# Kernel tuning notes

Measured on AMD Instinct MI355X. Metric: run time of the kernel, lower is better.

Reference implementation:

```python
import jax, jax.numpy as jnp
import numpy as np

N = 50000      # nodes
E = 800000     # edges
NF = 16        # nfeature_dim
H = 128        # hidden_dim
OUT = 4        # output_dim


def _edge_conv(x, edge_index, W1, b1, W2, b2, aggr):
    """PyG EdgeConv: message = MLP(cat[x_i, x_j - x_i]) per edge, aggregate at target i.
    edge_index[0]=source j, edge_index[1]=target i."""
    src, dst = edge_index[0], edge_index[1]
    xi = x[dst]                                   # [E, F]
    xj = x[src]                                   # [E, F]
    h = jnp.concatenate([xi, xj - xi], axis=-1)   # [E, 2F]
    m = jax.nn.relu(h @ W1 + b1) @ W2 + b2        # [E, H]
    if aggr == 'max':
        out = jax.ops.segment_max(m, dst, num_segments=N)
        out = jnp.where(jnp.isfinite(out), out, 0.0)  # nodes with no in-edges -> 0
    else:  # mean
        s = jax.ops.segment_sum(m, dst, num_segments=N)
        cnt = jax.ops.segment_sum(jnp.ones((m.shape[0], 1), m.dtype), dst, num_segments=N)
        out = s / jnp.maximum(cnt, 1.0)
    return out


def setup_inputs() -> dict:
    key = jax.random.key(0)
    ks = jax.random.split(key, 20)
    s = 0.05
    inp = {
        'x': jax.random.normal(ks[0], (N, NF), dtype=jnp.float32),
        'edge_attr': jax.random.uniform(ks[1], (E, 1), dtype=jnp.float32) + 0.1,
        'edge_index': jax.random.randint(ks[2], (2, E), 0, N, dtype=jnp.int64),
        # conv0: Linear(2*NF->H), Linear(H->H)
        'W01': jax.random.normal(ks[3], (2 * NF, H), dtype=jnp.float32) * s,
        'b01': jnp.zeros((H,), jnp.float32),
        'W02': jax.random.normal(ks[4], (H, H), dtype=jnp.float32) * s,
        'b02': jnp.zeros((H,), jnp.float32),
        # conv1: Linear(2*H->H), Linear(H->H)
        'W11': jax.random.normal(ks[5], (2 * H, H), dtype=jnp.float32) * s,
        'b11': jnp.zeros((H,), jnp.float32),
        'W12': jax.random.normal(ks[6], (H, H), dtype=jnp.float32) * s,
        'b12': jnp.zeros((H,), jnp.float32),
        # conv2: Linear(2*H->H), Linear(H->H)
        'W21': jax.random.normal(ks[7], (2 * H, H), dtype=jnp.float32) * s,
        'b21': jnp.zeros((H,), jnp.float32),
        'W22': jax.random.normal(ks[8], (H, H), dtype=jnp.float32) * s,
        'b22': jnp.zeros((H,), jnp.float32),
        # final fc
        'Wf': jax.random.normal(ks[9], (H, OUT), dtype=jnp.float32) * s,
        'bf': jnp.zeros((OUT,), jnp.float32),
    }
    return inp


def reference(x, edge_attr, edge_index, W01, b01, W02, b02, W11, b11, W12, b12,
              W21, b21, W22, b22, Wf, bf):
    # edge_attr is only nan-checked in the original forward; unused in math.
    # dropout_rate = 0.0 -> identity (eval-mode reference).
    h = _edge_conv(x, edge_index, W01, b01, W02, b02, 'max')
    h = jax.nn.relu(h)
    h = _edge_conv(h, edge_index, W11, b11, W12, b12, 'mean')
    h = jax.nn.relu(h)
    h = _edge_conv(h, edge_index, W21, b21, W22, b22, 'mean')
    return h @ Wf + bf  # [N, OUT]
```

## Files before the change

### kernel.cpp

```cpp
#include <hip/hip_runtime.h>
#include <stdint.h>

#define NNODES 50000
#define NEDGES 800000
#define FDIM 16
#define HDIM 128
#define NPAD 50176
#define NCH 98
#define NBLK64 782

typedef __attribute__((ext_vector_type(8))) short short8;
typedef __attribute__((ext_vector_type(4))) float f32x4;

static constexpr size_t NH  = (size_t)NNODES * HDIM;
static constexpr size_t NHB = NH * sizeof(float);

static constexpr size_t OFF_ENC   = 0;
static constexpr size_t OFF_PA    = NHB;
static constexpr size_t OFF_PB    = OFF_PA + NH * 2;
static constexpr size_t OFF_QA    = OFF_PB + NH * 2;
static constexpr size_t OFF_QB    = OFF_QA + NH * 2;
static constexpr size_t OFF_CNT   = OFF_QB + NH * 2;
static constexpr size_t OFF_CUR   = OFF_CNT + NPAD * 4;
static constexpr size_t OFF_CSUM  = OFF_CUR + NPAD * 4;
static constexpr size_t OFF_COFF  = OFF_CSUM + 512;
static constexpr size_t OFF_WFOLD = OFF_COFF + 512;
static constexpr size_t OFF_BFOLD = OFF_WFOLD + 2048;
static constexpr size_t OFF_FLAG  = OFF_BFOLD + 256;
static constexpr size_t OFF_SEDGE = OFF_FLAG + 256;
static constexpr size_t OFF_W02H  = OFF_SEDGE + (size_t)NEDGES * 8;
static constexpr size_t OFF_W02L  = OFF_W02H + 32768;
static constexpr size_t OFF_W12H  = OFF_W02L + 32768;
static constexpr size_t OFF_W12L  = OFF_W12H + 32768;
static constexpr size_t OFF_W11H  = OFF_W12L + 32768;
static constexpr size_t OFF_W11L  = OFF_W11H + 65536;
static constexpr size_t OFF_W21H  = OFF_W11L + 65536;
static constexpr size_t OFF_W21L  = OFF_W21H + 65536;

__device__ inline unsigned enc_f32(float m) {
  unsigned u = __float_as_uint(m);
  return (u & 0x80000000u) ? ~u : (u | 0x80000000u);
}

__device__ inline ushort bf16_rne(float v) {
  const unsigned u = __float_as_uint(v);
  return (ushort)((u + 0x7fffu + ((u >> 16) & 1u)) >> 16);
}

__device__ inline void bf16_split(float v, ushort& h, ushort& l) {
  unsigned u = __float_as_uint(v);
  unsigned hb = (u + 0x7fffu + ((u >> 16) & 1u)) & 0xffff0000u;
  h = (ushort)(hb >> 16);
  float r = v - __uint_as_float(hb);
  unsigned ur = __float_as_uint(r);
  l = (ushort)((ur + 0x7fffu + ((ur >> 16) & 1u)) >> 16);
}

__device__ inline short8 cvtpk8_bf16(const float v[8]) {
  unsigned r[4];
  #pragma unroll
  for (int k = 0; k < 4; ++k)
    asm("v_cvt_pk_bf16_f32 %0, %1, %2" : "=v"(r[k]) : "v"(v[2 * k]), "v"(v[2 * k + 1]));
  return *(short8*)r;
}

__device__ inline unsigned cvtpk_bf16(float a, float b) {
  unsigned r;
  asm("v_cvt_pk_bf16_f32 %0, %1, %2" : "=v"(r) : "v"(a), "v"(b));
  return r;
}

__global__ __launch_bounds__(256) void k_init(const int* __restrict__ raw,
                                              int* __restrict__ flag,
                                              unsigned* __restrict__ cnt,
                                              unsigned* __restrict__ outenc) {
  const int i = blockIdx.x * 256 + threadIdx.x;
  outenc[i] = 0u;
  if (i < NPAD) cnt[i] = 0u;
  if (i == 0) {
    int is64 = 1;
    #pragma unroll
    for (int k = 1; k < 64; k += 2)
      if (raw[k] != 0) is64 = 0;
    *flag = is64;
  }
}

__global__ __launch_bounds__(256) void k_count(const int* __restrict__ raw,
                                               const int* __restrict__ flag,
                                               unsigned* __restrict__ cnt) {
  const size_t e = (size_t)blockIdx.x * 256 + threadIdx.x;
  const int d = (*flag) ? raw[2 * ((size_t)NEDGES + e)] : raw[NEDGES + e];
  atomicAdd(&cnt[d], 1u);
}

__global__ __launch_bounds__(256) void k_scan1(const unsigned* __restrict__ cnt,
                                               unsigned* __restrict__ csum) {
  __shared__ unsigned s[256];
  const int t = threadIdx.x, b = blockIdx.x;
  s[t] = cnt[b * 512 + t] + cnt[b * 512 + 256 + t];
  __syncthreads();
  for (int off = 128; off; off >>= 1) {
    if (t < off) s[t] += s[t + off];
    __syncthreads();
  }
  if (t == 0) csum[b] = s[0];
}

__global__ void k_scan2(const unsigned* __restrict__ csum,
                        unsigned* __restrict__ coff) {
  if (threadIdx.x == 0) {
    unsigned r = 0;
    for (int i = 0; i < NCH; ++i) { coff[i] = r; r += csum[i]; }
  }
}

__global__ __launch_bounds__(256) void k_scan3(const unsigned* __restrict__ cnt,
                                               const unsigned* __restrict__ coff,
                                               unsigned* __restrict__ cursor) {
  __shared__ unsigned s[256];
  const int t = threadIdx.x, b = blockIdx.x;
  const int base = b * 512;
  const unsigned c0 = cnt[base + 2 * t], c1 = cnt[base + 2 * t + 1];
  s[t] = c0 + c1;
  __syncthreads();
  for (int off = 1; off < 256; off <<= 1) {
    unsigned v = s[t];
    if (t >= off) v += s[t - off];
    __syncthreads();
    s[t] = v;
    __syncthreads();
  }
  const unsigned o = coff[b] + s[t] - (c0 + c1);
  cursor[base + 2 * t] = o;
  cursor[base + 2 * t + 1] = o + c0;
}

__global__ __launch_bounds__(256) void k_scatter(const int* __restrict__ raw,
                                                 const int* __restrict__ flag,
                                                 unsigned* __restrict__ cursor,
                                                 int2* __restrict__ sedge) {
  const size_t e = (size_t)blockIdx.x * 256 + threadIdx.x;
  int s, d;
  if (*flag) { s = raw[2 * e]; d = raw[2 * ((size_t)NEDGES + e)]; }
  else       { s = raw[e];     d = raw[NEDGES + e]; }
  const unsigned p = atomicAdd(&cursor[d], 1u);
  int2 sd; sd.x = s; sd.y = d;
  sedge[p] = sd;
}

__device__ inline void prepw_body(const float* __restrict__ W2,
                                  ushort* __restrict__ Whi,
                                  ushort* __restrict__ Wlo, int blk) {
  const int gid = blk * 256 + threadIdx.x;
  const int row = gid & 15;
  const int kg  = (gid >> 4) & 3;
  const int ks  = (gid >> 6) & 3;
  const int ct  = gid >> 8;
  const int col = ct * 16 + row;
  const int k0  = ks * 32 + kg * 8;
  short8 hv, lv;
  #pragma unroll
  for (int j = 0; j < 8; ++j) {
    ushort h, l;
    bf16_split(W2[(size_t)(k0 + j) * HDIM + col], h, l);
    hv[j] = (short)h; lv[j] = (short)l;
  }
  *(short8*)(Whi + (size_t)gid * 8) = hv;
  *(short8*)(Wlo + (size_t)gid * 8) = lv;
}

__device__ inline void packab_body(const float* __restrict__ W1,
                                   ushort* __restrict__ Whi,
                                   ushort* __restrict__ Wlo, int blk) {
  const int gid = blk * 256 + threadIdx.x;
  const int row = gid & 15;
  const int kg  = (gid >> 4) & 3;
  const int ks  = (gid >> 6) & 3;
  const int ct  = gid >> 8;
  const int col = ct * 16 + row;
  const int k0  = ks * 32 + kg * 8;
  short8 hv, lv;
  #pragma unroll
  for (int j = 0; j < 8; ++j) {
    const int k = k0 + j;
    float v;
    if (col < HDIM) v = W1[(size_t)k * HDIM + col] - W1[(size_t)(k + HDIM) * HDIM + col];
    else            v = W1[(size_t)(k + HDIM) * HDIM + (col - HDIM)];
    ushort h, l;
    bf16_split(v, h, l);
    hv[j] = (short)h; lv[j] = (short)l;
  }
  *(short8*)(Whi + (size_t)gid * 8) = hv;
  *(short8*)(Wlo + (size_t)gid * 8) = lv;
}

__global__ __launch_bounds__(256) void k_prep_all(
    const float* __restrict__ W02, const float* __restrict__ W12,
    const float* __restrict__ W11, const float* __restrict__ W21,
    const float* __restrict__ W22, const float* __restrict__ Wf,
    const float* __restrict__ b22, const float* __restrict__ bf,
    ushort* __restrict__ W02h, ushort* __restrict__ W02l,
    ushort* __restrict__ W12h, ushort* __restrict__ W12l,
    ushort* __restrict__ W11h, ushort* __restrict__ W11l,
    ushort* __restrict__ W21h, ushort* __restrict__ W21l,
    float* __restrict__ Wfold, float* __restrict__ bfold) {
  const int b = blockIdx.x;
  if (b < 8)       prepw_body(W02, W02h, W02l, b);
  else if (b < 16) prepw_body(W12, W12h, W12l, b - 8);
  else if (b < 32) packab_body(W11, W11h, W11l, b - 16);
  else if (b < 48) packab_body(W21, W21h, W21l, b - 32);
  else {
    const int t = (b - 48) * 256 + threadIdx.x;
    const int f = t >> 2, o = t & 3;
    float acc = 0.f;
    for (int h = 0; h < HDIM; ++h)
      acc = fmaf(W22[f * HDIM + h], Wf[h * 4 + o], acc);
    Wfold[t] = acc;
    if (t < 4) {
      float a = bf[t];
      for (int h = 0; h < HDIM; ++h) a = fmaf(b22[h], Wf[h * 4 + t], a);
      bfold[t] = a;
    }
  }
}

__global__ __launch_bounds__(256) void k_node_ab16(const float* __restrict__ x,
                                                   const float* __restrict__ W1,
                                                   const float* __restrict__ b1,
                                                   ushort* __restrict__ Ab,
                                                   ushort* __restrict__ Bb) {
  __shared__ float s_x[16 * FDIM];
  const int tid = threadIdx.x;
  const int nb = blockIdx.x * 16;
  s_x[tid] = x[(size_t)nb * FDIM + tid];
  __syncthreads();
  const int h = tid & 127;
  const int half = tid >> 7;
  float accA[8], accB[8];
  #pragma unroll
  for (int j = 0; j < 8; ++j) { accA[j] = 0.f; accB[j] = 0.f; }
  #pragma unroll 4
  for (int f = 0; f < FDIM; ++f) {
    const float wt = W1[f * HDIM + h];
    const float wb = W1[(f + FDIM) * HDIM + h];
    const float wd = wt - wb;
    #pragma unroll
    for (int j = 0; j < 8; ++j) {
      const float xv = s_x[(half * 8 + j) * FDIM + f];
      accA[j] = fmaf(xv, wd, accA[j]);
      accB[j] = fmaf(xv, wb, accB[j]);
    }
  }
  const float bias = b1[h];
  #pragma unroll
  for (int j = 0; j < 8; ++j) {
    const size_t idx = (size_t)(nb + half * 8 + j) * HDIM + h;
    Ab[idx] = bf16_rne(accA[j] + bias);
    Bb[idx] = bf16_rne(accB[j]);
  }
}

__global__ __launch_bounds__(256) void k_node_ab_mfma(
    const unsigned* __restrict__ X, const ushort* __restrict__ Whi,
    const ushort* __restrict__ Wlo, const float* __restrict__ b1,
    ushort* __restrict__ Ab, ushort* __restrict__ Bb) {
  __shared__ __align__(16) ushort s_t[64 * 128];
  const int tid = threadIdx.x;
  const int nb = blockIdx.x * 64;

  #pragma unroll
  for (int it = 0; it < 4; ++it) {
    const int idx = tid + it * 256;
    const int row = idx >> 4;
    const int kg8 = idx & 15;
    const int n = nb + row;
    float v[8];
    if (n < NNODES) {
      const unsigned* p = X + (size_t)n * HDIM + kg8 * 8;
      const uint4 u0 = *(const uint4*)p;
      const uint4 u1 = *(const uint4*)(p + 4);
      const unsigned uu[8] = {u0.x, u0.y, u0.z, u0.w, u1.x, u1.y, u1.z, u1.w};
      #pragma unroll
      for (int j = 0; j < 8; ++j)
        v[j] = (uu[j] & 0x80000000u) ? __uint_as_float(uu[j] ^ 0x80000000u) : 0.f;
    } else {
      #pragma unroll
      for (int j = 0; j < 8; ++j) v[j] = 0.f;
    }
    const short8 hv = cvtpk8_bf16(v);
    const int unit = row * 16 + (kg8 ^ (row & 15));
    *(short8*)(s_t + unit * 8) = hv;
  }
  __syncthreads();

  const int l15 = tid & 15;
  const int l4  = (tid >> 4) & 3;
  const int w   = tid >> 6;

  f32x4 acc[4][4];
  #pragma unroll
  for (int rt = 0; rt < 4; ++rt)
    #pragma unroll
    for (int c = 0; c < 4; ++c)
      #pragma unroll
      for (int r = 0; r < 4; ++r) acc[rt][c][r] = 0.f;

  #pragma unroll
  for (int ks = 0; ks < 4; ++ks) {
    short8 wh[4], wl[4];
    #pragma unroll
    for (int ctl = 0; ctl < 4; ++ctl) {
      const int ct_g = w * 4 + ctl;
      const size_t u = ((size_t)(((ct_g * 4 + ks) * 4 + l4) * 16 + l15)) * 8;
      wh[ctl] = *(const short8*)(Whi + u);
      wl[ctl] = *(const short8*)(Wlo + u);
    }
    #pragma unroll
    for (int rt = 0; rt < 4; ++rt) {
      const int unit = (rt * 16 + l15) * 16 + ((ks * 4 + l4) ^ l15);
      const short8 ah = *(const short8*)(s_t + unit * 8);
      #pragma unroll
      for (int ctl = 0; ctl < 4; ++ctl) {
        acc[rt][ctl] = __builtin_amdgcn_mfma_f32_16x16x32_bf16(ah, wl[ctl], acc[rt][ctl], 0, 0, 0);
        acc[rt][ctl] = __builtin_amdgcn_mfma_f32_16x16x32_bf16(ah, wh[ctl], acc[rt][ctl], 0, 0, 0);
      }
    }
  }

  #pragma unroll
  for (int ctl = 0; ctl < 4; ++ctl) {
    const int col_g = w * 64 + ctl * 16 + l15;
    if (col_g < HDIM) {
      const float bias = b1[col_g];
      #pragma unroll
      for (int rt = 0; rt < 4; ++rt)
        #pragma unroll
        for (int r = 0; r < 4; ++r) {
          const int n = nb + rt * 16 + l4 * 4 + r;
          if (n < NNODES) Ab[(size_t)n * HDIM + col_g] = bf16_rne(acc[rt][ctl][r] + bias);
        }
    } else {
      const int cb = col_g - HDIM;
      #pragma unroll
      for (int rt = 0; rt < 4; ++rt)
        #pragma unroll
        for (int r = 0; r < 4; ++r) {
          const int n = nb + rt * 16 + l4 * 4 + r;
          if (n < NNODES) Bb[(size_t)n * HDIM + cb] = bf16_rne(acc[rt][ctl][r]);
        }
    }
  }
}

__global__ __launch_bounds__(256) void k_l2_mega(
    const ushort* __restrict__ A1, const ushort* __restrict__ B1,
    const int2* __restrict__ sedge, const unsigned* __restrict__ endv,
    const unsigned* __restrict__ cnt,
    const ushort* __restrict__ W12h, const ushort* __restrict__ W12l,
    const float* __restrict__ b12,
    const ushort* __restrict__ W21h, const ushort* __restrict__ W21l,
    const float* __restrict__ b21,
    ushort* __restrict__ A2, ushort* __restrict__ B2) {
  __shared__ __align__(16) ushort s_t[64 * 128];
  __shared__ float s_m[64 * 132];
  __shared__ float s_scale[64];
  __shared__ float s_alive[64];
  const int tid = threadIdx.x;
  const int nb = blockIdx.x * 64;
  if (tid < 64) {
    const int n = nb + tid;
    const unsigned c = (n < NNODES) ? cnt[n] : 0u;
    s_scale[tid] = c ? 1.f / (float)c : 0.f;
    s_alive[tid] = c ? 1.f : 0.f;
  }
  __syncthreads();

  const int w    = tid >> 6;
  const int lane = tid & 63;

  for (int ln = 0; ln < 16; ++ln) {
    const int row = w * 16 + ln;
    const int n = nb + row;
    float sx = 0.f, sy = 0.f;
    float ax = 0.f, ay = 0.f;
    unsigned deg = 0, end = 0;
    if (n < NNODES) {
      deg = cnt[n];
      end = endv[n];
      const unsigned a_dw = *(const unsigned*)(A1 + (size_t)n * HDIM + lane * 2);
      ax = __uint_as_float(a_dw << 16);
      ay = __uint_as_float(a_dw & 0xffff0000u);
    }
    const unsigned start = end - deg;
    for (unsigned cb = start; cb < end; cb += 64) {
      const int m = (int)((end - cb < 64u) ? (end - cb) : 64u);
      int myidx = 0;
      if (lane < m) myidx = sedge[cb + lane].x;
      int k = 0;
      for (; k + 8 <= m; k += 8) {
        unsigned bv[8];
        #pragma unroll
        for (int j = 0; j < 8; ++j) {
          const int id = __shfl(myidx, k + j);
          bv[j] = *(const unsigned*)(B1 + (size_t)id * HDIM + lane * 2);
        }
        #pragma unroll
        for (int j = 0; j < 8; ++j) {
          sx += fmaxf(ax + __uint_as_float(bv[j] << 16), 0.f);
          sy += fmaxf(ay + __uint_as_float(bv[j] & 0xffff0000u), 0.f);
        }
      }
      for (; k < m; ++k) {
        const int id = __shfl(myidx, k);
        const unsigned bv = *(const unsigned*)(B1 + (size_t)id * HDIM + lane * 2);
        sx += fmaxf(ax + __uint_as_float(bv << 16), 0.f);
        sy += fmaxf(ay + __uint_as_float(bv & 0xffff0000u), 0.f);
      }
    }
    const float sc = s_scale[row];
    const unsigned pk = cvtpk_bf16(sx * sc, sy * sc);
    const int unit = row * 16 + ((lane >> 2) ^ (row & 15));
    *(unsigned*)((char*)s_t + unit * 16 + (lane & 3) * 4) = pk;
  }
  __syncthreads();

  const int l15 = tid & 15;
  const int l4  = (tid >> 4) & 3;

  {
    f32x4 acc[4][2];
    #pragma unroll
    for (int rt = 0; rt < 4; ++rt)
      #pragma unroll
      for (int c = 0; c < 2; ++c)
        #pragma unroll
        for (int r = 0; r < 4; ++r) acc[rt][c][r] = 0.f;

    #pragma unroll
    for (int ks = 0; ks < 4; ++ks) {
      short8 wh[2], wl[2];
      #pragma unroll
      for (int ctl = 0; ctl < 2; ++ctl) {
        const int ct_g = w * 2 + ctl;
        const size_t u = ((size_t)(((ct_g * 4 + ks) * 4 + l4) * 16 + l15)) * 8;
        wh[ctl] = *(const short8*)(W12h + u);
        wl[ctl] = *(const short8*)(W12l + u);
      }
      #pragma unroll
      for (int rt = 0; rt < 4; ++rt) {
        const int unit = (rt * 16 + l15) * 16 + ((ks * 4 + l4) ^ l15);
        const short8 ah = *(const short8*)(s_t + unit * 8);
        #pragma unroll
        for (int ctl = 0; ctl < 2; ++ctl) {
          acc[rt][ctl] = __builtin_amdgcn_mfma_f32_16x16x32_bf16(ah, wl[ctl], acc[rt][ctl], 0, 0, 0);
          acc[rt][ctl] = __builtin_amdgcn_mfma_f32_16x16x32_bf16(ah, wh[ctl], acc[rt][ctl], 0, 0, 0);
        }
      }
    }

    const float bb0 = b12[w * 32 + l15];
    const float bb1 = b12[w * 32 + 16 + l15];
    #pragma unroll
    for (int rt = 0; rt < 4; ++rt)
      #pragma unroll
      for (int ctl = 0; ctl < 2; ++ctl)
        #pragma unroll
        for (int r = 0; r < 4; ++r) {
          const int row = rt * 16 + l4 * 4 + r;
          s_m[row * 132 + w * 32 + ctl * 16 + l15] =
              fmaxf(acc[rt][ctl][r] + (ctl ? bb1 : bb0), 0.f) * s_alive[row];
        }
  }
  __syncthreads();

  #pragma unroll
  for (int it = 0; it < 4; ++it) {
    const int idx = tid + it * 256;
    const int row = idx >> 4;
    const int kg8 = idx & 15;
    const float* p = s_m + row * 132 + kg8 * 8;
    float v[8];
    const float4 a0 = *(const float4*)p;
    const float4 a1 = *(const float4*)(p + 4);
    v[0] = a0.x; v[1] = a0.y; v[2] = a0.z; v[3] = a0.w;
    v[4] = a1.x; v[5] = a1.y; v[6] = a1.z; v[7] = a1.w;
    const short8 hv = cvtpk8_bf16(v);
    const int unit = row * 16 + (kg8 ^ (row & 15));
    *(short8*)(s_t + unit * 8) = hv;
  }
  __syncthreads();

  f32x4 acc2[4][4];
  #pragma unroll
  for (int rt = 0; rt < 4; ++rt)
    #pragma unroll
    for (int c = 0; c < 4; ++c)
      #pragma unroll
      for (int r = 0; r < 4; ++r) acc2[rt][c][r] = 0.f;

  #pragma unroll
  for (int ks = 0; ks < 4; ++ks) {
    short8 wh[4], wl[4];
    #pragma unroll
    for (int ctl = 0; ctl < 4; ++ctl) {
      const int ct_g = w * 4 + ctl;
      const size_t u = ((size_t)(((ct_g * 4 + ks) * 4 + l4) * 16 + l15)) * 8;
      wh[ctl] = *(const short8*)(W21h + u);
      wl[ctl] = *(const short8*)(W21l + u);
    }
    #pragma unroll
    for (int rt = 0; rt < 4; ++rt) {
      const int unit = (rt * 16 + l15) * 16 + ((ks * 4 + l4) ^ l15);
      const short8 ah = *(const short8*)(s_t + unit * 8);
      #pragma unroll
      for (int ctl = 0; ctl < 4; ++ctl) {
        acc2[rt][ctl] = __builtin_amdgcn_mfma_f32_16x16x32_bf16(ah, wl[ctl], acc2[rt][ctl], 0, 0, 0);
        acc2[rt][ctl] = __builtin_amdgcn_mfma_f32_16x16x32_bf16(ah, wh[ctl], acc2[rt][ctl], 0, 0, 0);
      }
    }
  }

  #pragma unroll
  for (int ctl = 0; ctl < 4; ++ctl) {
    const int col_g = w * 64 + ctl * 16 + l15;
    if (col_g < HDIM) {
      const float bias = b21[col_g];
      #pragma unroll
      for (int rt = 0; rt < 4; ++rt)
        #pragma unroll
        for (int r = 0; r < 4; ++r) {
          const int n = nb + rt * 16 + l4 * 4 + r;
          if (n < NNODES) A2[(size_t)n * HDIM + col_g] = bf16_rne(acc2[rt][ctl][r] + bias);
        }
    } else {
      const int cb = col_g - HDIM;
      #pragma unroll
      for (int rt = 0; rt < 4; ++rt)
        #pragma unroll
        for (int r = 0; r < 4; ++r) {
          const int n = nb + rt * 16 + l4 * 4 + r;
          if (n < NNODES) B2[(size_t)n * HDIM + cb] = bf16_rne(acc2[rt][ctl][r]);
        }
    }
  }
}

__global__ __launch_bounds__(256) void k_edge_l0_mfma(
    const ushort* __restrict__ A0b, const ushort* __restrict__ B0b,
    const int2* __restrict__ sedge,
    const ushort* __restrict__ Whi,
    const float* __restrict__ b2, unsigned* __restrict__ outenc) {
  __shared__ __align__(16) char s_un[4 * 64 * 17 * 4];
  __shared__ int s_dstA[64];
  __shared__ int s_srcA[64];
  ushort* s_t = (ushort*)s_un;
  float*  s_m = (float*)s_un;

  const int tid = threadIdx.x;
  const int eb = blockIdx.x * 64;
  if (tid < 64) {
    const int2 sd = sedge[eb + tid];
    s_srcA[tid] = sd.x;
    s_dstA[tid] = sd.y;
  }
  __syncthreads();

  #pragma unroll
  for (int it = 0; it < 4; ++it) {
    const int idx = tid + it * 256;
    const int e = idx >> 4;
    const int kg8 = idx & 15;
    const int k0 = kg8 * 8;
    const short8 a8 = *(const short8*)(A0b + (size_t)s_dstA[e] * HDIM + k0);
    const short8 b8 = *(const short8*)(B0b + (size_t)s_srcA[e] * HDIM + k0);
    float v[8];
    #pragma unroll
    for (int j = 0; j < 8; ++j) {
      const float av = __uint_as_float(((unsigned)(ushort)a8[j]) << 16);
      const float bv = __uint_as_float(((unsigned)(ushort)b8[j]) << 16);
      v[j] = fmaxf(av + bv, 0.f);
    }
    const short8 hv = cvtpk8_bf16(v);
    const int unit = e * 16 + (kg8 ^ (e & 15));
    *(short8*)(s_t + unit * 8) = hv;
  }
  __syncthreads();

  const int l15 = tid & 15;
  const int l4  = (tid >> 4) & 3;
  const int w   = tid >> 6;

  f32x4 acc[4][2];
  #pragma unroll
  for (int rt = 0; rt < 4; ++rt)
    #pragma unroll
    for (int c = 0; c < 2; ++c)
      #pragma unroll
      for (int r = 0; r < 4; ++r) acc[rt][c][r] = 0.f;

  #pragma unroll
  for (int ks = 0; ks < 4; ++ks) {
    short8 wh[2];
    #pragma unroll
    for (int ctl = 0; ctl < 2; ++ctl) {
      const int ct_g = w * 2 + ctl;
      const size_t u = ((size_t)(((ct_g * 4 + ks) * 4 + l4) * 16 + l15)) * 8;
      wh[ctl] = *(const short8*)(Whi + u);
    }
    #pragma unroll
    for (int rt = 0; rt < 4; ++rt) {
      const int e = rt * 16 + l15;
      const int unit = e * 16 + ((ks * 4 + l4) ^ l15);
      const short8 ah = *(const short8*)(s_t + unit * 8);
      #pragma unroll
      for (int ctl = 0; ctl < 2; ++ctl)
        acc[rt][ctl] = __builtin_amdgcn_mfma_f32_16x16x32_bf16(ah, wh[ctl], acc[rt][ctl], 0, 0, 0);
    }
  }
  __syncthreads();

  float* smw = s_m + w * (64 * 17);
  const int le = tid & 63;
  const int colw = le & 15;
  const int g = le >> 4;
  const int e0 = g * 16;
  int dd[16];
  #pragma unroll
  for (int e = 0; e < 16; ++e) dd[e] = s_dstA[e0 + e];
  #pragma unroll
  for (int ctl = 0; ctl < 2; ++ctl) {
    const float bb = b2[w * 32 + ctl * 16 + l15];
    #pragma unroll
    for (int rt = 0; rt < 4; ++rt)
      #pragma unroll
      for (int r = 0; r < 4; ++r)
        smw[(rt * 16 + l4 * 4 + r) * 17 + l15] = acc[rt][ctl][r] + bb;
    float vv[16];
    #pragma unroll
    for (int e = 0; e < 16; ++e) vv[e] = smw[(e0 + e) * 17 + colw];
    unsigned* const ocol = outenc + w * 32 + ctl * 16 + colw;
    int curd = dd[0];
    float run = vv[0];
    #pragma unroll
    for (int e = 1; e < 16; ++e) {
      const bool same = (dd[e] == curd);
      if (!same) atomicMax(ocol + (size_t)curd * HDIM, enc_f32(run));
      run = same ? fmaxf(run, vv[e]) : vv[e];
      curd = dd[e];
    }
    atomicMax(ocol + (size_t)curd * HDIM, enc_f32(run));
  }
}

__global__ __launch_bounds__(256) void k_seg_final(const ushort* __restrict__ A,
                                                   const ushort* __restrict__ B,
                                                   const int2* __restrict__ sedge,
                                                   const unsigned* __restrict__ endv,
                                                   const unsigned* __restrict__ cnt,
                                                   const float* __restrict__ Wfold,
                                                   const float* __restrict__ bfold,
                                                   const float* __restrict__ bf,
                                                   float* __restrict__ out) {
  const int tid = threadIdx.x;
  const int n = blockIdx.x * 4 + (tid >> 6);
  const int lane = tid & 63;
  const unsigned deg = cnt[n];
  if (deg == 0) {
    if (lane == 0) {
      float4 o; o.x = bf[0]; o.y = bf[1]; o.z = bf[2]; o.w = bf[3];
      ((float4*)out)[n] = o;
    }
    return;
  }
  const unsigned end = endv[n];
  const unsigned start = end - deg;
  const unsigned a_dw = *(const unsigned*)(A + (size_t)n * HDIM + lane * 2);
  const float ax = __uint_as_float(a_dw << 16);
  const float ay = __uint_as_float(a_dw & 0xffff0000u);
  float sx = 0.f, sy = 0.f;
  for (unsigned cb = start; cb < end; cb += 64) {
    const int m = (int)((end - cb < 64u) ? (end - cb) : 64u);
    int myidx = 0;
    if (lane < m) myidx = sedge[cb + lane].x;
    int k = 0;
    for (; k + 8 <= m; k += 8) {
      unsigned bv[8];
      #pragma unroll
      for (int j = 0; j < 8; ++j) {
        const int id = __shfl(myidx, k + j);
        bv[j] = *(const unsigned*)(B + (size_t)id * HDIM + lane * 2);
      }
      #pragma unroll
      for (int j = 0; j < 8; ++j) {
        sx += fmaxf(ax + __uint_as_float(bv[j] << 16), 0.f);
        sy += fmaxf(ay + __uint_as_float(bv[j] & 0xffff0000u), 0.f);
      }
    }
    for (; k < m; ++k) {
      const int id = __shfl(myidx, k);
      const unsigned bv = *(const unsigned*)(B + (size_t)id * HDIM + lane * 2);
      sx += fmaxf(ax + __uint_as_float(bv << 16), 0.f);
      sy += fmaxf(ay + __uint_as_float(bv & 0xffff0000u), 0.f);
    }
  }
  const float inv = 1.f / (float)deg;
  const float vx = sx * inv, vy = sy * inv;
  const float4 w0 = ((const float4*)Wfold)[lane * 2];
  const float4 w1 = ((const float4*)Wfold)[lane * 2 + 1];
  float p0 = fmaf(vx, w0.x, vy * w1.x);
  float p1 = fmaf(vx, w0.y, vy * w1.y);
  float p2 = fmaf(vx, w0.z, vy * w1.z);
  float p3 = fmaf(vx, w0.w, vy * w1.w);
  #pragma unroll
  for (int off = 32; off; off >>= 1) {
    p0 += __shfl_xor(p0, off);
    p1 += __shfl_xor(p1, off);
    p2 += __shfl_xor(p2, off);
    p3 += __shfl_xor(p3, off);
  }
  if (lane == 0) {
    float4 o;
    o.x = p0 + bfold[0]; o.y = p1 + bfold[1];
    o.z = p2 + bfold[2]; o.w = p3 + bfold[3];
    ((float4*)out)[n] = o;
  }
}

extern "C" void kernel_launch(void* const* d_in, const int* in_sizes, int n_in,
                              void* d_out, int out_size, void* d_ws, size_t ws_size,
                              hipStream_t stream) {
  const float* x   = (const float*)d_in[0];
  const int*   eidx = (const int*)d_in[2];
  const float* W01 = (const float*)d_in[3];
  const float* b01 = (const float*)d_in[4];
  const float* W02 = (const float*)d_in[5];
  const float* b02 = (const float*)d_in[6];
  const float* W11 = (const float*)d_in[7];
  const float* b11 = (const float*)d_in[8];
  const float* W12 = (const float*)d_in[9];
  const float* b12 = (const float*)d_in[10];
  const float* W21 = (const float*)d_in[11];
  const float* b21 = (const float*)d_in[12];
  const float* W22 = (const float*)d_in[13];
  const float* b22 = (const float*)d_in[14];
  const float* Wf  = (const float*)d_in[15];
  const float* bf  = (const float*)d_in[16];
  float* out = (float*)d_out;
  char* ws = (char*)d_ws;

  unsigned* enc = (unsigned*)(ws + OFF_ENC);
  ushort* PA = (ushort*)(ws + OFF_PA);
  ushort* PB = (ushort*)(ws + OFF_PB);
  ushort* QA = (ushort*)(ws + OFF_QA);
  ushort* QB = (ushort*)(ws + OFF_QB);
  unsigned* cnt    = (unsigned*)(ws + OFF_CNT);
  unsigned* cursor = (unsigned*)(ws + OFF_CUR);
  unsigned* csum   = (unsigned*)(ws + OFF_CSUM);
  unsigned* coff   = (unsigned*)(ws + OFF_COFF);
  float* Wfold = (float*)(ws + OFF_WFOLD);
  float* bfold = (float*)(ws + OFF_BFOLD);
  int* flag  = (int*)(ws + OFF_FLAG);
  int2* sedge = (int2*)(ws + OFF_SEDGE);
  ushort* W02h = (ushort*)(ws + OFF_W02H);
  ushort* W02l = (ushort*)(ws + OFF_W02L);
  ushort* W12h = (ushort*)(ws + OFF_W12H);
  ushort* W12l = (ushort*)(ws + OFF_W12L);
  ushort* W11h = (ushort*)(ws + OFF_W11H);
  ushort* W11l = (ushort*)(ws + OFF_W11L);
  ushort* W21h = (ushort*)(ws + OFF_W21H);
  ushort* W21l = (ushort*)(ws + OFF_W21L);

  k_init<<<(int)(NH / 256), 256, 0, stream>>>(eidx, flag, cnt, enc);
  k_count<<<NEDGES / 256, 256, 0, stream>>>(eidx, flag, cnt);
  k_scan1<<<NCH, 256, 0, stream>>>(cnt, csum);
  k_scan2<<<1, 64, 0, stream>>>(csum, coff);
  k_scan3<<<NCH, 256, 0, stream>>>(cnt, coff, cursor);
  k_scatter<<<NEDGES / 256, 256, 0, stream>>>(eidx, flag, cursor, sedge);
  k_prep_all<<<50, 256, 0, stream>>>(W02, W12, W11, W21, W22, Wf, b22, bf,
                                     W02h, W02l, W12h, W12l, W11h, W11l,
                                     W21h, W21l, Wfold, bfold);

  k_node_ab16<<<NNODES / 16, 256, 0, stream>>>(x, W01, b01, PA, PB);
  k_edge_l0_mfma<<<NEDGES / 64, 256, 0, stream>>>(PA, PB, sedge, W02h, b02, enc);

  k_node_ab_mfma<<<NBLK64, 256, 0, stream>>>(enc, W11h, W11l, b11, QA, QB);

  k_l2_mega<<<NBLK64, 256, 0, stream>>>(QA, QB, sedge, cursor, cnt,
                                        W12h, W12l, b12, W21h, W21l, b21,
                                        PA, PB);

  k_seg_final<<<NNODES / 4, 256, 0, stream>>>(PA, PB, sedge, cursor, cnt,
                                              Wfold, bfold, bf, out);

  (void)in_sizes; (void)n_in; (void)out_size; (void)ws_size;
}
```

Baseline: 476.5 us.

## Split layer-2 mega kernel into per-node segment-mean and MFMA node kernel

```diff
diff --git a/kernel.cpp b/kernel.cpp
--- a/kernel.cpp
+++ b/kernel.cpp
@@ -353,10 +353,53 @@
   }
 }
 
-__global__ __launch_bounds__(256) void k_l2_mega(
-    const ushort* __restrict__ A1, const ushort* __restrict__ B1,
-    const int2* __restrict__ sedge, const unsigned* __restrict__ endv,
-    const unsigned* __restrict__ cnt,
+__global__ __launch_bounds__(256) void k_seg_mean(const ushort* __restrict__ A,
+                                                  const ushort* __restrict__ B,
+                                                  const int2* __restrict__ sedge,
+                                                  const unsigned* __restrict__ endv,
+                                                  const unsigned* __restrict__ cnt,
+                                                  ushort* __restrict__ Sb) {
+  const int tid = threadIdx.x;
+  const int n = blockIdx.x * 4 + (tid >> 6);
+  const int lane = tid & 63;
+  const unsigned deg = cnt[n];
+  const unsigned end = endv[n];
+  const unsigned start = end - deg;
+  const unsigned a_dw = *(const unsigned*)(A + (size_t)n * HDIM + lane * 2);
+  const float ax = __uint_as_float(a_dw << 16);
+  const float ay = __uint_as_float(a_dw & 0xffff0000u);
+  float sx = 0.f, sy = 0.f;
+  for (unsigned cb = start; cb < end; cb += 64) {
+    const int m = (int)((end - cb < 64u) ? (end - cb) : 64u);
+    int myidx = 0;
+    if (lane < m) myidx = sedge[cb + lane].x;
+    int k = 0;
+    for (; k + 8 <= m; k += 8) {
+      unsigned bv[8];
+      #pragma unroll
+      for (int j = 0; j < 8; ++j) {
+        const int id = __shfl(myidx, k + j);
+        bv[j] = *(const unsigned*)(B + (size_t)id * HDIM + lane * 2);
+      }
+      #pragma unroll
+      for (int j = 0; j < 8; ++j) {
+        sx += fmaxf(ax + __uint_as_float(bv[j] << 16), 0.f);
+        sy += fmaxf(ay + __uint_as_float(bv[j] & 0xffff0000u), 0.f);
+      }
+    }
+    for (; k < m; ++k) {
+      const int id = __shfl(myidx, k);
+      const unsigned bv = *(const unsigned*)(B + (size_t)id * HDIM + lane * 2);
+      sx += fmaxf(ax + __uint_as_float(bv << 16), 0.f);
+      sy += fmaxf(ay + __uint_as_float(bv & 0xffff0000u), 0.f);
+    }
+  }
+  const float sc = deg ? 1.f / (float)deg : 0.f;
+  *(unsigned*)(Sb + (size_t)n * HDIM + lane * 2) = cvtpk_bf16(sx * sc, sy * sc);
+}
+
+__global__ __launch_bounds__(256) void k_node_l2_fused(
+    const ushort* __restrict__ Sb, const unsigned* __restrict__ cnt,
     const ushort* __restrict__ W12h, const ushort* __restrict__ W12l,
     const float* __restrict__ b12,
     const ushort* __restrict__ W21h, const ushort* __restrict__ W21l,
@@ -364,69 +407,35 @@
     ushort* __restrict__ A2, ushort* __restrict__ B2) {
   __shared__ __align__(16) ushort s_t[64 * 128];
   __shared__ float s_m[64 * 132];
-  __shared__ float s_scale[64];
   __shared__ float s_alive[64];
   const int tid = threadIdx.x;
   const int nb = blockIdx.x * 64;
   if (tid < 64) {
     const int n = nb + tid;
     const unsigned c = (n < NNODES) ? cnt[n] : 0u;
-    s_scale[tid] = c ? 1.f / (float)c : 0.f;
     s_alive[tid] = c ? 1.f : 0.f;
   }
-  __syncthreads();
-
-  const int w    = tid >> 6;
-  const int lane = tid & 63;
-
-  for (int ln = 0; ln < 16; ++ln) {
-    const int row = w * 16 + ln;
+
+  #pragma unroll
+  for (int it = 0; it < 4; ++it) {
+    const int idx = tid + it * 256;
+    const int row = idx >> 4;
+    const int kg8 = idx & 15;
     const int n = nb + row;
-    float sx = 0.f, sy = 0.f;
-    float ax = 0.f, ay = 0.f;
-    unsigned deg = 0, end = 0;
-    if (n < NNODES) {
-      deg = cnt[n];
-      end = endv[n];
-      const unsigned a_dw = *(const unsigned*)(A1 + (size_t)n * HDIM + lane * 2);
-      ax = __uint_as_float(a_dw << 16);
-      ay = __uint_as_float(a_dw & 0xffff0000u);
-    }
-    const unsigned start = end - deg;
-    for (unsigned cb = start; cb < end; cb += 64) {
-      const int m = (int)((end - cb < 64u) ? (end - cb) : 64u);
-      int myidx = 0;
-      if (lane < m) myidx = sedge[cb + lane].x;
-      int k = 0;
-      for (; k + 8 <= m; k += 8) {
-        unsigned bv[8];
-        #pragma unroll
-        for (int j = 0; j < 8; ++j) {
-          const int id = __shfl(myidx, k + j);
-          bv[j] = *(const unsigned*)(B1 + (size_t)id * HDIM + lane * 2);
-        }
-        #pragma unroll
-        for (int j = 0; j < 8; ++j) {
-          sx += fmaxf(ax + __uint_as_float(bv[j] << 16), 0.f);
-          sy += fmaxf(ay + __uint_as_float(bv[j] & 0xffff0000u), 0.f);
-        }
-      }
-      for (; k < m; ++k) {
-        const int id = __shfl(myidx, k);
-        const unsigned bv = *(const unsigned*)(B1 + (size_t)id * HDIM + lane * 2);
-        sx += fmaxf(ax + __uint_as_float(bv << 16), 0.f);
-        sy += fmaxf(ay + __uint_as_float(bv & 0xffff0000u), 0.f);
-      }
-    }
-    const float sc = s_scale[row];
-    const unsigned pk = cvtpk_bf16(sx * sc, sy * sc);
-    const int unit = row * 16 + ((lane >> 2) ^ (row & 15));
-    *(unsigned*)((char*)s_t + unit * 16 + (lane & 3) * 4) = pk;
+    short8 hv;
+    if (n < NNODES) hv = *(const short8*)(Sb + (size_t)n * HDIM + kg8 * 8);
+    else {
+      #pragma unroll
+      for (int j = 0; j < 8; ++j) hv[j] = 0;
+    }
+    const int unit = row * 16 + (kg8 ^ (row & 15));
+    *(short8*)(s_t + unit * 8) = hv;
   }
   __syncthreads();
 
   const int l15 = tid & 15;
   const int l4  = (tid >> 4) & 3;
+  const int w   = tid >> 6;
 
   {
     f32x4 acc[4][2];
@@ -750,6 +759,7 @@
   char* ws = (char*)d_ws;
 
   unsigned* enc = (unsigned*)(ws + OFF_ENC);
+  ushort* Sb = (ushort*)(ws + OFF_ENC);
   ushort* PA = (ushort*)(ws + OFF_PA);
   ushort* PB = (ushort*)(ws + OFF_PB);
   ushort* QA = (ushort*)(ws + OFF_QA);
@@ -785,11 +795,10 @@
   k_edge_l0_mfma<<<NEDGES / 64, 256, 0, stream>>>(PA, PB, sedge, W02h, b02, enc);
 
   k_node_ab_mfma<<<NBLK64, 256, 0, stream>>>(enc, W11h, W11l, b11, QA, QB);
-
-  k_l2_mega<<<NBLK64, 256, 0, stream>>>(QA, QB, sedge, cursor, cnt,
-                                        W12h, W12l, b12, W21h, W21l, b21,
-                                        PA, PB);
-
+  k_seg_mean<<<NNODES / 4, 256, 0, stream>>>(QA, QB, sedge, cursor, cnt, Sb);
+
+  k_node_l2_fused<<<NBLK64, 256, 0, stream>>>(Sb, cnt, W12h, W12l, b12,
+                                              W21h, W21l, b21, PA, PB);
   k_seg_final<<<NNODES / 4, 256, 0, stream>>>(PA, PB, sedge, cursor, cnt,
                                               Wfold, bfold, bf, out);
 
```

New measurement: 419.9 us. -11.9%, faster.
